# Kernel optimization log

Hardware: AMD Instinct MI355X
Metric: run time of the kernel (lower is better)

The kernel has to match this reference:

```python
import jax, jax.numpy as jnp
import numpy as np

VOCAB = 30000
K1 = 1.2
B_PARAM = 0.75


def setup_inputs() -> dict:
    key = jax.random.key(0)
    k1, k2 = jax.random.split(key)
    B, L = 2048, 512
    input_ids = jax.random.randint(k1, (B, L), 0, VOCAB, dtype=jnp.int64)
    attention_mask = jnp.ones((B, L), dtype=jnp.int64)
    W = jax.random.normal(k2, (768, VOCAB), dtype=jnp.float32) / np.sqrt(VOCAB)
    return {"input_ids": input_ids, "attention_mask": attention_mask, "W": W}


def reference(input_ids, attention_mask, W):
    B, L = input_ids.shape
    # valid tokens: attended AND 100 < id < VOCAB
    valid = (attention_mask == 1) & (input_ids > 100) & (input_ids < VOCAB)
    validf = valid.astype(jnp.float32)
    doc_len = validf.sum(-1)  # [B]

    # batched histogram (TF counts) via scatter-add; invalid entries add 0 at slot 0
    rows = jnp.broadcast_to(jnp.arange(B)[:, None], (B, L))
    toks = jnp.where(valid, input_ids, 0)
    tf = jnp.zeros((B, VOCAB), jnp.float32).at[rows, toks].add(validf)  # [B, VOCAB]

    # BM25 scoring; torch writes scores only at unique tokens -> equivalent to masking tf>0
    length_norm = jnp.maximum(1.0 + B_PARAM * (doc_len / 100.0 - 1.0), 0.5)[:, None]
    scores = jnp.where(tf > 0, tf * (K1 + 1.0) / (tf + K1 * length_norm), 0.0)

    v = scores + 1e-10
    v = v / jnp.linalg.norm(v, axis=-1, keepdims=True)  # F.normalize p=2

    out = v @ W.T  # Linear(VOCAB, 768, bias=False)
    out = out / jnp.linalg.norm(out, axis=-1, keepdims=True)
    return out
```

## Files before the change

### kernel.cpp

```cpp
#include <hip/hip_runtime.h>
#include <hip/hip_bf16.h>
#include <stdint.h>

#define B_ROWS 2048
#define SEQ 512
#define VOC 30000
#define DMODEL 768
#define K1 1.2f
#define BPAR 0.75f
#define NT 192
#define PF 8
#define TGX 235
#define TGY 12
#define TTILES (TGX * TGY)
#define NBLK (TTILES + B_ROWS)

__launch_bounds__(256)
__global__ void prep_trans(const float* __restrict__ W, __hip_bfloat16* __restrict__ Wb,
                           const int* __restrict__ ids, const int* __restrict__ mask,
                           int* __restrict__ stoks_g, float* __restrict__ wts_g,
                           int* __restrict__ n_g) {
    __shared__ ushort smem[64 * 130];
    uint32_t bid = blockIdx.x;
    int tid = threadIdx.x;

    uint32_t a  = bid * (uint32_t)B_ROWS / (uint32_t)NBLK;
    uint32_t b2 = (bid + 1u) * (uint32_t)B_ROWS / (uint32_t)NBLK;

    if (b2 == a) {
        ushort (*tile)[130] = (ushort(*)[130])smem;
        int tb = (int)(bid - a);
        int bx = tb % TGX, by = tb / TGX;
        int tBase = bx * 128;
        int jBase = by * 64;
        int tx = tid & 63;
        int ty = tid >> 6;

#pragma unroll
        for (int jj = 0; jj < 16; jj++) {
            int j = jBase + jj * 4 + ty;
            int t = tBase + tx * 2;
            if (t < VOC) {
                float2 v = *(const float2*)(W + (size_t)j * VOC + t);
                ushort2 u;
                u.x = __bfloat16_as_ushort(__float2bfloat16(v.x));
                u.y = __bfloat16_as_ushort(__float2bfloat16(v.y));
                *(ushort2*)&tile[jj * 4 + ty][tx * 2] = u;
            }
        }
        __syncthreads();

#pragma unroll
        for (int i = 0; i < 32; i++) {
            int trow = i * 4 + ty;
            int t = tBase + trow;
            if (t < VOC) {
                ((ushort*)Wb)[(size_t)t * DMODEL + jBase + tx] = tile[tx][trow];
            }
        }
    } else {
        int b = (int)a;
        int*   stoks = (int*)smem;
        float* wts   = (float*)((char*)smem + 2048);
        int*   nvp   = (int*)((char*)smem + 4096);

        if (tid == 0) *nvp = 0;
        __syncthreads();

        for (int i = tid; i < SEQ; i += 256) {
            int id = ids[(size_t)b * SEQ + i];
            int m  = mask[(size_t)b * SEQ + i];
            if (m == 1 && id > 100 && id < VOC) {
                stoks[atomicAdd(nvp, 1)] = id;
            }
        }
        __syncthreads();
        int n = *nvp;

        for (int i = n + tid; i < SEQ; i += 256) stoks[i] = 0x7fffffff;

        for (int k = 2; k <= SEQ; k <<= 1) {
            for (int j = k >> 1; j > 0; j >>= 1) {
                __syncthreads();
                for (int i = tid; i < SEQ; i += 256) {
                    int ixj = i ^ j;
                    if (ixj > i) {
                        int va = stoks[i], vc = stoks[ixj];
                        if ((va > vc) == ((i & k) == 0)) { stoks[i] = vc; stoks[ixj] = va; }
                    }
                }
            }
        }
        __syncthreads();

        float kln = K1 * fmaxf(1.0f + BPAR * ((float)n / 100.0f - 1.0f), 0.5f);
        for (int i = tid; i < n; i += 256) {
            int t = stoks[i];
            int lo = i; while (lo > 0 && stoks[lo - 1] == t) lo--;
            int hi = i; while (hi < n - 1 && stoks[hi + 1] == t) hi++;
            wts[i] = (K1 + 1.0f) / ((float)(hi - lo + 1) + kln);
        }
        __syncthreads();

        for (int i = tid; i < n; i += 256) {
            stoks_g[(size_t)b * SEQ + i] = stoks[i] * (DMODEL / 4);
            wts_g[(size_t)b * SEQ + i]   = wts[i];
        }
        if (tid == 0) n_g[b] = n;
    }
}

__device__ __forceinline__ float b2f(unsigned short h) {
    union { uint32_t u; float f; } v; v.u = ((uint32_t)h) << 16; return v.f;
}

__launch_bounds__(NT, 6)
__global__ void bm25_gather(const int* __restrict__ stoks_g, const float* __restrict__ wts_g,
                            const int* __restrict__ n_g,
                            const __hip_bfloat16* __restrict__ Wb,
                            float* __restrict__ out) {
    __shared__ int   stoks[SEQ];
    __shared__ float wts[SEQ];
    __shared__ float wred[3];

    int b = blockIdx.x;
    int tid = threadIdx.x;
    int n = n_g[b];

    for (int i = tid; i < n; i += NT) {
        stoks[i] = stoks_g[(size_t)b * SEQ + i];
        wts[i]   = wts_g[(size_t)b * SEQ + i];
    }
    __syncthreads();

    const ushort4* __restrict__ Wb4 = (const ushort4*)Wb;
    float4 acc = make_float4(0.f, 0.f, 0.f, 0.f);
    int p = 0;
    for (; p + PF <= n; p += PF) {
        ushort4 r[PF];
        float   w[PF];
#pragma unroll
        for (int q = 0; q < PF; q++) {
            r[q] = Wb4[(size_t)stoks[p + q] + tid];
            w[q] = wts[p + q];
        }
#pragma unroll
        for (int q = 0; q < PF; q++) {
            acc.x = fmaf(w[q], b2f(r[q].x), acc.x);
            acc.y = fmaf(w[q], b2f(r[q].y), acc.y);
            acc.z = fmaf(w[q], b2f(r[q].z), acc.z);
            acc.w = fmaf(w[q], b2f(r[q].w), acc.w);
        }
    }
    for (; p < n; p++) {
        float w = wts[p];
        ushort4 r = Wb4[(size_t)stoks[p] + tid];
        acc.x = fmaf(w, b2f(r.x), acc.x);
        acc.y = fmaf(w, b2f(r.y), acc.y);
        acc.z = fmaf(w, b2f(r.z), acc.z);
        acc.w = fmaf(w, b2f(r.w), acc.w);
    }

    float ss = acc.x * acc.x + acc.y * acc.y + acc.z * acc.z + acc.w * acc.w;
#pragma unroll
    for (int off = 32; off > 0; off >>= 1) ss += __shfl_down(ss, off);
    if ((tid & 63) == 0) wred[tid >> 6] = ss;
    __syncthreads();
    float inv = rsqrtf(fmaxf(wred[0] + wred[1] + wred[2], 1e-30f));

    float4 o;
    o.x = acc.x * inv; o.y = acc.y * inv; o.z = acc.z * inv; o.w = acc.w * inv;
    ((float4*)(out + (size_t)b * DMODEL))[tid] = o;
}

extern "C" void kernel_launch(void* const* d_in, const int* in_sizes, int n_in,
                              void* d_out, int out_size, void* d_ws, size_t ws_size,
                              hipStream_t stream) {
    const int*   ids  = (const int*)d_in[0];
    const int*   mask = (const int*)d_in[1];
    const float* W    = (const float*)d_in[2];
    float* out = (float*)d_out;

    char* ws = (char*)d_ws;
    __hip_bfloat16* Wb = (__hip_bfloat16*)ws;
    size_t off = (size_t)VOC * DMODEL * sizeof(__hip_bfloat16);
    int*   stoks_g = (int*)(ws + off);        off += (size_t)B_ROWS * SEQ * 4;
    float* wts_g   = (float*)(ws + off);      off += (size_t)B_ROWS * SEQ * 4;
    int*   n_g     = (int*)(ws + off);

    prep_trans<<<NBLK, 256, 0, stream>>>(W, Wb, ids, mask, stoks_g, wts_g, n_g);

    bm25_gather<<<B_ROWS, NT, 0, stream>>>(stoks_g, wts_g, n_g, Wb, out);
}
```

Before: 144.5 us.

## Split gather by vocab partition so concurrent blocks share W rows in cache

Each document's sorted tokens are split into eight vocabulary ranges, and a separate block gathers W rows for each (document, range) pair. Blocks launched together therefore touch a narrower slice of the transposed W table, which should improve L2/MALL reuse. Partial sums are stored as bf16 and reduced and normalized by a new combine kernel. This adds a third kernel launch, extra partial-sum traffic, and bf16 rounding of the partials, which costs some accuracy.

```diff
diff --git a/kernel.cpp b/kernel.cpp
--- a/kernel.cpp
+++ b/kernel.cpp
@@ -10,6 +10,8 @@
 #define BPAR 0.75f
 #define NT 192
 #define PF 8
+#define NPART 8
+#define PSIZE (VOC / NPART)
 #define TGX 235
 #define TGY 12
 #define TTILES (TGX * TGY)
@@ -19,8 +21,9 @@
 __global__ void prep_trans(const float* __restrict__ W, __hip_bfloat16* __restrict__ Wb,
                            const int* __restrict__ ids, const int* __restrict__ mask,
                            int* __restrict__ stoks_g, float* __restrict__ wts_g,
-                           int* __restrict__ n_g) {
+                           int* __restrict__ poff_g) {
     __shared__ ushort smem[64 * 130];
+    __shared__ int poff[NPART + 1];
     uint32_t bid = blockIdx.x;
     int tid = threadIdx.x;
 
@@ -100,13 +103,21 @@
             int hi = i; while (hi < n - 1 && stoks[hi + 1] == t) hi++;
             wts[i] = (K1 + 1.0f) / ((float)(hi - lo + 1) + kln);
         }
+
+        if (tid <= NPART) poff[tid] = (tid == 0) ? 0 : n;
+        __syncthreads();
+        for (int i = tid; i < n; i += 256) {
+            int cp = stoks[i] / PSIZE;
+            int pp = (i == 0) ? -1 : stoks[i - 1] / PSIZE;
+            for (int q = pp + 1; q <= cp; q++) if (q > 0) poff[q] = i;
+        }
         __syncthreads();
 
         for (int i = tid; i < n; i += 256) {
             stoks_g[(size_t)b * SEQ + i] = stoks[i] * (DMODEL / 4);
             wts_g[(size_t)b * SEQ + i]   = wts[i];
         }
-        if (tid == 0) n_g[b] = n;
+        if (tid <= NPART) poff_g[b * (NPART + 1) + tid] = poff[tid];
     }
 }
 
@@ -115,28 +126,31 @@
 }
 
 __launch_bounds__(NT, 6)
-__global__ void bm25_gather(const int* __restrict__ stoks_g, const float* __restrict__ wts_g,
-                            const int* __restrict__ n_g,
-                            const __hip_bfloat16* __restrict__ Wb,
-                            float* __restrict__ out) {
+__global__ void bm25_part(const int* __restrict__ stoks_g, const float* __restrict__ wts_g,
+                          const int* __restrict__ poff_g,
+                          const __hip_bfloat16* __restrict__ Wb,
+                          __hip_bfloat16* __restrict__ part_g) {
     __shared__ int   stoks[SEQ];
     __shared__ float wts[SEQ];
-    __shared__ float wred[3];
-
-    int b = blockIdx.x;
+
+    int part = blockIdx.x & (NPART - 1);
+    int doc  = blockIdx.x >> 3;
     int tid = threadIdx.x;
-    int n = n_g[b];
-
-    for (int i = tid; i < n; i += NT) {
-        stoks[i] = stoks_g[(size_t)b * SEQ + i];
-        wts[i]   = wts_g[(size_t)b * SEQ + i];
+
+    int lo = poff_g[doc * (NPART + 1) + part];
+    int hi = poff_g[doc * (NPART + 1) + part + 1];
+    int m = hi - lo;
+
+    for (int i = tid; i < m; i += NT) {
+        stoks[i] = stoks_g[(size_t)doc * SEQ + lo + i];
+        wts[i]   = wts_g[(size_t)doc * SEQ + lo + i];
     }
     __syncthreads();
 
     const ushort4* __restrict__ Wb4 = (const ushort4*)Wb;
     float4 acc = make_float4(0.f, 0.f, 0.f, 0.f);
     int p = 0;
-    for (; p + PF <= n; p += PF) {
+    for (; p + PF <= m; p += PF) {
         ushort4 r[PF];
         float   w[PF];
 #pragma unroll
@@ -152,7 +166,7 @@
             acc.w = fmaf(w[q], b2f(r[q].w), acc.w);
         }
     }
-    for (; p < n; p++) {
+    for (; p < m; p++) {
         float w = wts[p];
         ushort4 r = Wb4[(size_t)stoks[p] + tid];
         acc.x = fmaf(w, b2f(r.x), acc.x);
@@ -161,6 +175,31 @@
         acc.w = fmaf(w, b2f(r.w), acc.w);
     }
 
+    ushort4 o;
+    o.x = __bfloat16_as_ushort(__float2bfloat16(acc.x));
+    o.y = __bfloat16_as_ushort(__float2bfloat16(acc.y));
+    o.z = __bfloat16_as_ushort(__float2bfloat16(acc.z));
+    o.w = __bfloat16_as_ushort(__float2bfloat16(acc.w));
+    ((ushort4*)part_g)[((size_t)doc * NPART + part) * NT + tid] = o;
+}
+
+__launch_bounds__(NT)
+__global__ void bm25_combine(const __hip_bfloat16* __restrict__ part_g,
+                             float* __restrict__ out) {
+    __shared__ float wred[3];
+    int doc = blockIdx.x;
+    int tid = threadIdx.x;
+
+    float4 acc = make_float4(0.f, 0.f, 0.f, 0.f);
+#pragma unroll
+    for (int p = 0; p < NPART; p++) {
+        ushort4 r = ((const ushort4*)part_g)[((size_t)doc * NPART + p) * NT + tid];
+        acc.x += b2f(r.x);
+        acc.y += b2f(r.y);
+        acc.z += b2f(r.z);
+        acc.w += b2f(r.w);
+    }
+
     float ss = acc.x * acc.x + acc.y * acc.y + acc.z * acc.z + acc.w * acc.w;
 #pragma unroll
     for (int off = 32; off > 0; off >>= 1) ss += __shfl_down(ss, off);
@@ -170,7 +209,7 @@
 
     float4 o;
     o.x = acc.x * inv; o.y = acc.y * inv; o.z = acc.z * inv; o.w = acc.w * inv;
-    ((float4*)(out + (size_t)b * DMODEL))[tid] = o;
+    ((float4*)(out + (size_t)doc * DMODEL))[tid] = o;
 }
 
 extern "C" void kernel_launch(void* const* d_in, const int* in_sizes, int n_in,
@@ -186,9 +225,12 @@
     size_t off = (size_t)VOC * DMODEL * sizeof(__hip_bfloat16);
     int*   stoks_g = (int*)(ws + off);        off += (size_t)B_ROWS * SEQ * 4;
     float* wts_g   = (float*)(ws + off);      off += (size_t)B_ROWS * SEQ * 4;
-    int*   n_g     = (int*)(ws + off);
-
-    prep_trans<<<NBLK, 256, 0, stream>>>(W, Wb, ids, mask, stoks_g, wts_g, n_g);
-
-    bm25_gather<<<B_ROWS, NT, 0, stream>>>(stoks_g, wts_g, n_g, Wb, out);
-}
+    int*   poff_g  = (int*)(ws + off);        off += (size_t)B_ROWS * (NPART + 1) * 4;
+    __hip_bfloat16* part_g = (__hip_bfloat16*)(ws + off);
+
+    prep_trans<<<NBLK, 256, 0, stream>>>(W, Wb, ids, mask, stoks_g, wts_g, poff_g);
+
+    bm25_part<<<B_ROWS * NPART, NT, 0, stream>>>(stoks_g, wts_g, poff_g, Wb, part_g);
+
+    bm25_combine<<<B_ROWS, NT, 0, stream>>>(part_g, out);
+}
```

After: 146.8 us. Within noise of the previous version (+1.6%).
